# Kernel tuning notes

Hardware: AMD Instinct MI355X
Metric: run time of the kernel (lower is better)

## Reference

```python
import jax, jax.numpy as jnp
import numpy as np

C = 32                      # channels
DIMS = (8, 14, 18)          # basis_dim_per_atom for the 3 atom types
COUNTS = (8192, 8192, 4096) # number of atoms of each type


def setup_inputs() -> dict:
    key = jax.random.key(0)
    ks = iter(jax.random.split(key, 32))
    inp = {}
    N = sum(d * n for d, n in zip(DIMS, COUNTS))  # 253952 total basis rows
    inp["x"] = jax.random.normal(next(ks), (N, C), jnp.float32)
    c2 = C * C
    off = 0
    for t, (d, n) in enumerate(zip(DIMS, COUNTS)):
        rows = d * n
        # index array equivalent to the boolean atomic_number_mask for this type
        inp[f"idx{t}"] = jnp.arange(off, off + rows, dtype=jnp.int32)
        off += rows
        A = jax.random.normal(next(ks), (d, d), jnp.float32)
        inp[f"S{t}"] = 0.1 * (A + A.T)  # symmetric Coulomb/overlap matrix stand-in
        inp[f"W1_{t}"] = jax.random.normal(next(ks), (c2, c2), jnp.float32) * 0.03
        inp[f"b1_{t}"] = jnp.zeros((c2,), jnp.float32)
        inp[f"g{t}"] = jnp.ones((c2,), jnp.float32)
        inp[f"beta{t}"] = jnp.zeros((c2,), jnp.float32)
        inp[f"W2_{t}"] = jax.random.normal(next(ks), (c2, c2), jnp.float32) * 0.03
        inp[f"b2_{t}"] = jnp.zeros((c2,), jnp.float32)
    return inp


def _atom_block(y, S, W1, b1, g, beta, W2, b2):
    # y: [n_atoms, d, C]
    n = y.shape[0]
    # l2 = einsum('ij,aic,ajm->acm', S, y, y)  -> [n, C, C]
    Sy = jnp.einsum('ij,ajm->aim', S, y)
    l2 = jnp.einsum('aic,aim->acm', y, Sy)
    h = l2.reshape(n, C * C)
    # MLP: Linear -> SiLU -> LayerNorm -> Linear
    h = jax.nn.silu(h @ W1.T + b1)
    mu = jnp.mean(h, axis=-1, keepdims=True)
    var = jnp.var(h, axis=-1, keepdims=True)
    h = (h - mu) * jax.lax.rsqrt(var + 1e-5) * g + beta
    l2 = (h @ W2.T + b2).reshape(n, C, C)
    # x = x @ l2 per atom
    return jnp.einsum('aic,acm->aim', y, l2)


def reference(x, idx0, idx1, idx2,
              S0, W1_0, b1_0, g0, beta0, W2_0, b2_0,
              S1, W1_1, b1_1, g1, beta1, W2_1, b2_1,
              S2, W1_2, b1_2, g2, beta2, W2_2, b2_2):
    idxs = (idx0, idx1, idx2)
    params = ((S0, W1_0, b1_0, g0, beta0, W2_0, b2_0),
              (S1, W1_1, b1_1, g1, beta1, W2_1, b2_1),
              (S2, W1_2, b1_2, g2, beta2, W2_2, b2_2))
    for t in range(3):  # fixed small loop over atom types (structurally distinct)
        d = DIMS[t]
        y = x[idxs[t]].reshape(-1, d, C)          # gather + view per atom
        out = _atom_block(y, *params[t])          # per-type sub-module
        x = x.at[idxs[t]].set(out.reshape(-1, C)) # scatter back
    return x
```

## Files before the change

### kernel.cpp

```cpp
#include <hip/hip_runtime.h>
#include <math.h>

#define C2 1024

typedef float f32x4 __attribute__((ext_vector_type(4)));
typedef _Float16 f16x8 __attribute__((ext_vector_type(8)));
typedef unsigned short u16x8 __attribute__((ext_vector_type(8)));

__device__ __forceinline__ unsigned short f2h(float f) {
    _Float16 h = (_Float16)f;
    return __builtin_bit_cast(unsigned short, h);
}
__device__ __forceinline__ float h2f(unsigned short u) {
    return (float)__builtin_bit_cast(_Float16, u);
}

__device__ __forceinline__ void gload16(const void* g, void* l) {
    __builtin_amdgcn_global_load_lds((const __attribute__((address_space(1))) void*)g,
                                     (__attribute__((address_space(3))) void*)l,
                                     16, 0, 0);
}

__device__ __forceinline__ int type_of(int pos, int s1, int s2) {
    return (pos >= s2) ? 2 : (pos >= s1) ? 1 : 0;
}
__device__ __forceinline__ int dim_of(int t) { return (t == 0) ? 8 : (t == 1) ? 14 : 18; }

__global__ __launch_bounds__(256) void k_conv(const float* __restrict__ s0, const float* __restrict__ s1,
                                              const float* __restrict__ s2, const float* __restrict__ s3,
                                              const float* __restrict__ s4, const float* __restrict__ s5,
                                              unsigned short* __restrict__ w) {
    int mat = blockIdx.x >> 10, bb = blockIdx.x & 1023;
    const float* src = (mat == 0) ? s0 : (mat == 1) ? s1 : (mat == 2) ? s2
                       : (mat == 3) ? s3 : (mat == 4) ? s4 : s5;
    int i = (bb * 256 + threadIdx.x) * 4;
    unsigned short* dst = w + (size_t)mat * 1048576;
    float4 v = *(const float4*)(src + i);
    ushort4 h;
    h.x = f2h(v.x); h.y = f2h(v.y); h.z = f2h(v.z); h.w = f2h(v.w);
    *(ushort4*)(dst + i) = h;
}

__global__ __launch_bounds__(256) void k_l2(const float* __restrict__ x,
                                            const int* __restrict__ i0, const int* __restrict__ i1,
                                            const int* __restrict__ i2,
                                            const float* __restrict__ S0, const float* __restrict__ S1,
                                            const float* __restrict__ S2,
                                            unsigned short* __restrict__ Ah,
                                            int s1, int s2) {
    __shared__ float sS[324];
    __shared__ float sy[4][18][32];
    __shared__ float sSy[4][18][32];
    const int tid = threadIdx.x, g = tid >> 6, lane = tid & 63;
    const int a0 = blockIdx.x * 4;
    const int t = type_of(a0, s1, s2);
    const int d = dim_of(t);
    const int* idx = (t == 0) ? i0 : (t == 1) ? i1 : i2;
    const float* S = (t == 0) ? S0 : (t == 1) ? S1 : S2;
    const int start = (t == 0) ? 0 : (t == 1) ? s1 : s2;
    const int dd = d * d;
    for (int i = tid; i < dd; i += 256) sS[i] = S[i];
    const int a = a0 + g, la = a - start;
    const int nf4 = d * 8;
    for (int k = lane; k < nf4; k += 64) {
        int bi = k >> 3, f4 = (k & 7) * 4;
        int r = idx[la * d + bi];
        *(float4*)&sy[g][bi][f4] = *(const float4*)(x + (size_t)r * 32 + f4);
    }
    __syncthreads();
    for (int k = lane; k < d * 32; k += 64) {
        int i = k >> 5, m = k & 31;
        float acc = 0.f;
        for (int j = 0; j < d; ++j) acc += sS[i * d + j] * sy[g][j][m];
        sSy[g][i][m] = acc;
    }
    __syncthreads();
    const int c = lane >> 1, mb = (lane & 1) * 16;
    float acc[16];
#pragma unroll
    for (int mm = 0; mm < 16; ++mm) acc[mm] = 0.f;
    for (int i = 0; i < d; ++i) {
        float yc = sy[g][i][c];
#pragma unroll
        for (int mm = 0; mm < 16; ++mm) acc[mm] += yc * sSy[g][i][mb + mm];
    }
    u16x8 h0, h1;
#pragma unroll
    for (int mm = 0; mm < 8; ++mm) h0[mm] = f2h(acc[mm]);
#pragma unroll
    for (int mm = 0; mm < 8; ++mm) h1[mm] = f2h(acc[8 + mm]);
    size_t off = (size_t)a * C2 + lane * 16;
    *(u16x8*)(Ah + off) = h0;
    *(u16x8*)(Ah + off + 8) = h1;
}

template <int DO_SILU>
__global__ __launch_bounds__(256) void k_gemm_mfma(const unsigned short* __restrict__ A,
                                                   const unsigned short* __restrict__ W0,
                                                   const unsigned short* __restrict__ W1,
                                                   const unsigned short* __restrict__ W2,
                                                   const float* __restrict__ bias0, const float* __restrict__ bias1,
                                                   const float* __restrict__ bias2,
                                                   unsigned short* __restrict__ Out, int tb1, int tb2) {
    __shared__ short lds[8704];
    short* As = lds;
    short* Ws = lds + 4096;

    const int tid = threadIdx.x;
    const int wid = tid >> 6, lane = tid & 63;
    const int bm = blockIdx.x, bn = blockIdx.y;
    const int wr = wid >> 1, wc = wid & 1;

    const unsigned short* W; const float* bias;
    if (bm >= tb2)      { W = W2; bias = bias2; }
    else if (bm >= tb1) { W = W1; bias = bias1; }
    else                { W = W0; bias = bias0; }

    size_t gA[2], gW[2];
    int ldsoff[2];
#pragma unroll
    for (int it = 0; it < 2; ++it) {
        int L = wid * 128 + it * 64 + lane;
        int row = L >> 2, slot = L & 3;
        int sw = slot ^ ((row >> 1) & 3);
        gA[it] = (size_t)(bm * 128 + row) * C2 + sw * 8;
        gW[it] = (size_t)(bn * 128 + row) * C2 + sw * 8;
        ldsoff[it] = wid * 1024 + it * 512;
    }

    const int col = lane & 15, g = lane >> 4;
    int aoffs[4], woffs[4];
#pragma unroll
    for (int i = 0; i < 4; ++i) {
        int ra = wr * 64 + i * 16 + col;
        aoffs[i] = ra * 32 + (g ^ ((ra >> 1) & 3)) * 8;
        int rw = wc * 64 + i * 16 + col;
        woffs[i] = rw * 32 + (g ^ ((rw >> 1) & 3)) * 8;
    }

    f32x4 acc[4][4] = {};

    for (int k0 = 0; k0 < C2; k0 += 32) {
#pragma unroll
        for (int it = 0; it < 2; ++it) {
            gload16(A + gA[it] + k0, As + ldsoff[it]);
            gload16(W + gW[it] + k0, Ws + ldsoff[it]);
        }
        __syncthreads();
        f16x8 ah[4], wh[4];
#pragma unroll
        for (int i = 0; i < 4; ++i) {
            ah[i] = *(const f16x8*)(As + aoffs[i]);
            wh[i] = *(const f16x8*)(Ws + woffs[i]);
        }
#pragma unroll
        for (int mi = 0; mi < 4; ++mi)
#pragma unroll
            for (int ni = 0; ni < 4; ++ni)
                acc[mi][ni] = __builtin_amdgcn_mfma_f32_16x16x32_f16(ah[mi], wh[ni], acc[mi][ni], 0, 0, 0);
        __syncthreads();
    }

    float bv[4];
#pragma unroll
    for (int ni = 0; ni < 4; ++ni) bv[ni] = bias[bn * 128 + wc * 64 + ni * 16 + col];

#pragma unroll
    for (int hp = 0; hp < 2; ++hp) {
        __syncthreads();
#pragma unroll
        for (int mh = 0; mh < 2; ++mh) {
            int mi = hp * 2 + mh;
#pragma unroll
            for (int ni = 0; ni < 4; ++ni)
#pragma unroll
                for (int r = 0; r < 4; ++r) {
                    float v = acc[mi][ni][r] + bv[ni];
                    if (DO_SILU) v = v / (1.f + __expf(-v));
                    int row = mh * 16 + g * 4 + r;
                    int colc = wc * 64 + ni * 16 + col;
                    lds[(wr * 32 + row) * 136 + colc] = (short)f2h(v);
                }
        }
        __syncthreads();
#pragma unroll
        for (int i = 0; i < 4; ++i) {
            int ci = tid + i * 256;
            int wrp = ci >> 9, rem = ci & 511;
            int row = rem >> 4, c8 = rem & 15;
            u16x8 val = *(u16x8*)&lds[(wrp * 32 + row) * 136 + c8 * 8];
            int grow = bm * 128 + wrp * 64 + hp * 32 + row;
            int gcol = bn * 128 + c8 * 8;
            *(u16x8*)&Out[(size_t)grow * C2 + gcol] = val;
        }
    }
}

__global__ __launch_bounds__(256) void k_ln(const unsigned short* __restrict__ H,
                                            const float* __restrict__ g0, const float* __restrict__ g1,
                                            const float* __restrict__ g2,
                                            const float* __restrict__ b0, const float* __restrict__ b1,
                                            const float* __restrict__ b2,
                                            unsigned short* __restrict__ Bh,
                                            int s1, int s2) {
    const int tid = threadIdx.x, w = tid >> 6, lane = tid & 63;
    const int row = blockIdx.x * 4 + w;
    const int t = type_of(row, s1, s2);
    const float* gg = (t == 0) ? g0 : (t == 1) ? g1 : g2;
    const float* bb = (t == 0) ? b0 : (t == 1) ? b1 : b2;
    const unsigned short* rp = H + (size_t)row * C2 + lane * 16;
    u16x8 hv0 = *(const u16x8*)rp;
    u16x8 hv1 = *(const u16x8*)(rp + 8);
    float v[16];
#pragma unroll
    for (int k = 0; k < 8; ++k) v[k] = h2f(hv0[k]);
#pragma unroll
    for (int k = 0; k < 8; ++k) v[8 + k] = h2f(hv1[k]);
    float s = 0.f, s2v = 0.f;
#pragma unroll
    for (int k = 0; k < 16; ++k) { s += v[k]; s2v += v[k] * v[k]; }
#pragma unroll
    for (int off = 1; off < 64; off <<= 1) {
        s += __shfl_xor(s, off);
        s2v += __shfl_xor(s2v, off);
    }
    float mean = s * (1.f / 1024.f);
    float var = s2v * (1.f / 1024.f) - mean * mean;
    float rstd = rsqrtf(var + 1e-5f);
    u16x8 o0, o1;
#pragma unroll
    for (int q = 0; q < 4; ++q) {
        float4 gv = *(const float4*)(gg + lane * 16 + q * 4);
        float4 bv = *(const float4*)(bb + lane * 16 + q * 4);
        float r0 = (v[q * 4 + 0] - mean) * rstd * gv.x + bv.x;
        float r1 = (v[q * 4 + 1] - mean) * rstd * gv.y + bv.y;
        float r2 = (v[q * 4 + 2] - mean) * rstd * gv.z + bv.z;
        float r3 = (v[q * 4 + 3] - mean) * rstd * gv.w + bv.w;
        if (q < 2) {
            o0[q * 4 + 0] = f2h(r0); o0[q * 4 + 1] = f2h(r1);
            o0[q * 4 + 2] = f2h(r2); o0[q * 4 + 3] = f2h(r3);
        } else {
            o1[(q - 2) * 4 + 0] = f2h(r0); o1[(q - 2) * 4 + 1] = f2h(r1);
            o1[(q - 2) * 4 + 2] = f2h(r2); o1[(q - 2) * 4 + 3] = f2h(r3);
        }
    }
    unsigned short* op = Bh + (size_t)row * C2 + lane * 16;
    *(u16x8*)op = o0;
    *(u16x8*)(op + 8) = o1;
}

__global__ __launch_bounds__(256) void k_out(const float* __restrict__ x,
                                             const int* __restrict__ i0, const int* __restrict__ i1,
                                             const int* __restrict__ i2,
                                             const unsigned short* __restrict__ L,
                                             float* __restrict__ out, int s1, int s2) {
    __shared__ float sL[4][C2];
    __shared__ float sy[4][18][32];
    const int tid = threadIdx.x, g = tid >> 6, lane = tid & 63;
    const int a0 = blockIdx.x * 4;
    const int t = type_of(a0, s1, s2);
    const int d = dim_of(t);
    const int* idx = (t == 0) ? i0 : (t == 1) ? i1 : i2;
    const int start = (t == 0) ? 0 : (t == 1) ? s1 : s2;
    const int a = a0 + g, la = a - start;
    for (int k = lane; k < 128; k += 64) {
        u16x8 hv = *(const u16x8*)(L + (size_t)a * C2 + k * 8);
#pragma unroll
        for (int q = 0; q < 8; ++q) sL[g][k * 8 + q] = h2f(hv[q]);
    }
    const int nf4 = d * 8;
    for (int k = lane; k < nf4; k += 64) {
        int bi = k >> 3, f4 = (k & 7) * 4;
        int r = idx[la * d + bi];
        *(float4*)&sy[g][bi][f4] = *(const float4*)(x + (size_t)r * 32 + f4);
    }
    __syncthreads();
    for (int k = lane; k < nf4; k += 64) {
        int bi = k >> 3, m4 = (k & 7) * 4;
        float ax = 0.f, ay = 0.f, az = 0.f, aw = 0.f;
#pragma unroll
        for (int c = 0; c < 32; ++c) {
            float yv = sy[g][bi][c];
            float4 lv = *(const float4*)&sL[g][c * 32 + m4];
            ax += yv * lv.x; ay += yv * lv.y; az += yv * lv.z; aw += yv * lv.w;
        }
        int r = idx[la * d + bi];
        float4 o = {ax, ay, az, aw};
        *(float4*)(out + (size_t)r * 32 + m4) = o;
    }
}

extern "C" void kernel_launch(void* const* d_in, const int* in_sizes, int n_in,
                              void* d_out, int out_size, void* d_ws, size_t ws_size,
                              hipStream_t stream) {
    const float* x = (const float*)d_in[0];
    static const int DIMS[3] = {8, 14, 18};
    static const int NATOMS[3] = {8192, 8192, 4096};
    const size_t MiB = 1ull << 20;
    const int BIG = 0x40000000;
    char* p = (char*)d_ws;

    const int* idxs[3]; const float* Ss[3]; const float* W1s[3]; const float* b1s[3];
    const float* gs[3]; const float* bes[3]; const float* W2s[3]; const float* b2s[3];
    for (int t = 0; t < 3; ++t) {
        idxs[t] = (const int*)d_in[1 + 8 * t];
        Ss[t] = (const float*)d_in[2 + 8 * t];
        W1s[t] = (const float*)d_in[3 + 8 * t];
        b1s[t] = (const float*)d_in[4 + 8 * t];
        gs[t] = (const float*)d_in[5 + 8 * t];
        bes[t] = (const float*)d_in[6 + 8 * t];
        W2s[t] = (const float*)d_in[7 + 8 * t];
        b2s[t] = (const float*)d_in[8 + 8 * t];
    }
    float* outp = (float*)d_out;

    if (ws_size >= 92 * MiB) {
        unsigned short* w = (unsigned short*)p;
        unsigned short* Ah = (unsigned short*)(p + 12 * MiB);
        unsigned short* H = (unsigned short*)(p + 52 * MiB);
        k_conv<<<6 * 1024, 256, 0, stream>>>(W1s[0], W2s[0], W1s[1], W2s[1], W1s[2], W2s[2], w);
        k_l2<<<5120, 256, 0, stream>>>(x, idxs[0], idxs[1], idxs[2], Ss[0], Ss[1], Ss[2],
                                       Ah, 8192, 16384);
        dim3 gg(160, 8);
        k_gemm_mfma<1><<<gg, 256, 0, stream>>>(Ah,
            w + 0 * 1048576, w + 2 * 1048576, w + 4 * 1048576,
            b1s[0], b1s[1], b1s[2], H, 64, 128);
        k_ln<<<5120, 256, 0, stream>>>(H, gs[0], gs[1], gs[2], bes[0], bes[1], bes[2],
                                       Ah, 8192, 16384);
        k_gemm_mfma<0><<<gg, 256, 0, stream>>>(Ah,
            w + 1 * 1048576, w + 3 * 1048576, w + 5 * 1048576,
            b2s[0], b2s[1], b2s[2], H, 64, 128);
        k_out<<<5120, 256, 0, stream>>>(x, idxs[0], idxs[1], idxs[2], H, outp, 8192, 16384);
    } else {
        unsigned short* wt = (unsigned short*)p;
        char* dyn = p + 4 * MiB;
        for (int t = 0; t < 3; ++t) {
            int n = NATOMS[t], d = DIMS[t];
            size_t fullneed = 4 * MiB + (size_t)n * 4096;
            int nch = (ws_size >= fullneed) ? 1 : 2;
            int cm = n / nch;
            unsigned short* Ah = (unsigned short*)dyn;
            unsigned short* Hbuf = (unsigned short*)(dyn + (size_t)cm * 2048);
            int ss1 = (t == 0) ? BIG : 0;
            int ss2 = (t == 2) ? 0 : BIG;
            k_conv<<<2 * 1024, 256, 0, stream>>>(W1s[t], W2s[t], W1s[t], W1s[t], W1s[t], W1s[t], wt);
            for (int ch = 0; ch < nch; ++ch) {
                const int* idxc = idxs[t] + (size_t)(ch * cm) * d;
                k_l2<<<cm / 4, 256, 0, stream>>>(x, idxc, idxc, idxc, Ss[t], Ss[t], Ss[t],
                                                 Ah, ss1, ss2);
                dim3 g1(cm / 128, 8);
                k_gemm_mfma<1><<<g1, 256, 0, stream>>>(Ah,
                    wt + 0, wt + 0, wt + 0,
                    b1s[t], b1s[t], b1s[t], Hbuf, BIG, BIG);
                k_ln<<<cm / 4, 256, 0, stream>>>(Hbuf, gs[t], gs[t], gs[t], bes[t], bes[t], bes[t],
                                                 Ah, ss1, ss2);
                k_gemm_mfma<0><<<g1, 256, 0, stream>>>(Ah,
                    wt + 1048576, wt + 1048576, wt + 1048576,
                    b2s[t], b2s[t], b2s[t], Hbuf, BIG, BIG);
                k_out<<<cm / 4, 256, 0, stream>>>(x, idxc, idxc, idxc, Hbuf, outp, ss1, ss2);
            }
        }
    }
    (void)in_sizes; (void)n_in; (void)out_size;
}
```

Measured before the change: 329.9 us.

## Double-buffer GEMM LDS tiles and fuse weight conversion into front kernel

```diff
diff --git a/kernel.cpp b/kernel.cpp
--- a/kernel.cpp
+++ b/kernel.cpp
@@ -26,33 +26,37 @@
 }
 __device__ __forceinline__ int dim_of(int t) { return (t == 0) ? 8 : (t == 1) ? 14 : 18; }
 
-__global__ __launch_bounds__(256) void k_conv(const float* __restrict__ s0, const float* __restrict__ s1,
-                                              const float* __restrict__ s2, const float* __restrict__ s3,
-                                              const float* __restrict__ s4, const float* __restrict__ s5,
-                                              unsigned short* __restrict__ w) {
-    int mat = blockIdx.x >> 10, bb = blockIdx.x & 1023;
-    const float* src = (mat == 0) ? s0 : (mat == 1) ? s1 : (mat == 2) ? s2
-                       : (mat == 3) ? s3 : (mat == 4) ? s4 : s5;
-    int i = (bb * 256 + threadIdx.x) * 4;
-    unsigned short* dst = w + (size_t)mat * 1048576;
-    float4 v = *(const float4*)(src + i);
-    ushort4 h;
-    h.x = f2h(v.x); h.y = f2h(v.y); h.z = f2h(v.z); h.w = f2h(v.w);
-    *(ushort4*)(dst + i) = h;
-}
-
-__global__ __launch_bounds__(256) void k_l2(const float* __restrict__ x,
-                                            const int* __restrict__ i0, const int* __restrict__ i1,
-                                            const int* __restrict__ i2,
-                                            const float* __restrict__ S0, const float* __restrict__ S1,
-                                            const float* __restrict__ S2,
-                                            unsigned short* __restrict__ Ah,
-                                            int s1, int s2) {
+__global__ __launch_bounds__(256) void k_front(const float* __restrict__ x,
+                                               const int* __restrict__ i0, const int* __restrict__ i1,
+                                               const int* __restrict__ i2,
+                                               const float* __restrict__ S0, const float* __restrict__ S1,
+                                               const float* __restrict__ S2,
+                                               unsigned short* __restrict__ Ah,
+                                               int s1, int s2,
+                                               const float* __restrict__ w0, const float* __restrict__ w1,
+                                               const float* __restrict__ w2, const float* __restrict__ w3,
+                                               const float* __restrict__ w4, const float* __restrict__ w5,
+                                               unsigned short* __restrict__ w,
+                                               int nconv) {
     __shared__ float sS[324];
     __shared__ float sy[4][18][32];
     __shared__ float sSy[4][18][32];
-    const int tid = threadIdx.x, g = tid >> 6, lane = tid & 63;
-    const int a0 = blockIdx.x * 4;
+    const int tid = threadIdx.x;
+    if ((int)blockIdx.x < nconv) {
+        int mat = blockIdx.x >> 10, bb = blockIdx.x & 1023;
+        const float* src = (mat == 0) ? w0 : (mat == 1) ? w1 : (mat == 2) ? w2
+                           : (mat == 3) ? w3 : (mat == 4) ? w4 : w5;
+        int i = (bb * 256 + tid) * 4;
+        unsigned short* dst = w + (size_t)mat * 1048576;
+        float4 v = *(const float4*)(src + i);
+        ushort4 h;
+        h.x = f2h(v.x); h.y = f2h(v.y); h.z = f2h(v.z); h.w = f2h(v.w);
+        *(ushort4*)(dst + i) = h;
+        return;
+    }
+    const int bid = blockIdx.x - nconv;
+    const int g = tid >> 6, lane = tid & 63;
+    const int a0 = bid * 4;
     const int t = type_of(a0, s1, s2);
     const int d = dim_of(t);
     const int* idx = (t == 0) ? i0 : (t == 1) ? i1 : i2;
@@ -102,9 +106,7 @@
                                                    const float* __restrict__ bias0, const float* __restrict__ bias1,
                                                    const float* __restrict__ bias2,
                                                    unsigned short* __restrict__ Out, int tb1, int tb2) {
-    __shared__ short lds[8704];
-    short* As = lds;
-    short* Ws = lds + 4096;
+    __shared__ short lds[16384];
 
     const int tid = threadIdx.x;
     const int wid = tid >> 6, lane = tid & 63;
@@ -140,18 +142,28 @@
 
     f32x4 acc[4][4] = {};
 
+#pragma unroll
+    for (int it = 0; it < 2; ++it) {
+        gload16(A + gA[it], lds + ldsoff[it]);
+        gload16(W + gW[it], lds + 4096 + ldsoff[it]);
+    }
+    __syncthreads();
+
+    int base = 0;
     for (int k0 = 0; k0 < C2; k0 += 32) {
-#pragma unroll
-        for (int it = 0; it < 2; ++it) {
-            gload16(A + gA[it] + k0, As + ldsoff[it]);
-            gload16(W + gW[it] + k0, Ws + ldsoff[it]);
-        }
-        __syncthreads();
+        int nbase = base ^ 8192;
+        if (k0 + 32 < C2) {
+#pragma unroll
+            for (int it = 0; it < 2; ++it) {
+                gload16(A + gA[it] + k0 + 32, lds + nbase + ldsoff[it]);
+                gload16(W + gW[it] + k0 + 32, lds + nbase + 4096 + ldsoff[it]);
+            }
+        }
         f16x8 ah[4], wh[4];
 #pragma unroll
         for (int i = 0; i < 4; ++i) {
-            ah[i] = *(const f16x8*)(As + aoffs[i]);
-            wh[i] = *(const f16x8*)(Ws + woffs[i]);
+            ah[i] = *(const f16x8*)(lds + base + aoffs[i]);
+            wh[i] = *(const f16x8*)(lds + base + 4096 + woffs[i]);
         }
 #pragma unroll
         for (int mi = 0; mi < 4; ++mi)
@@ -159,6 +171,7 @@
             for (int ni = 0; ni < 4; ++ni)
                 acc[mi][ni] = __builtin_amdgcn_mfma_f32_16x16x32_f16(ah[mi], wh[ni], acc[mi][ni], 0, 0, 0);
         __syncthreads();
+        base = nbase;
     }
 
     float bv[4];
@@ -318,9 +331,10 @@
         unsigned short* w = (unsigned short*)p;
         unsigned short* Ah = (unsigned short*)(p + 12 * MiB);
         unsigned short* H = (unsigned short*)(p + 52 * MiB);
-        k_conv<<<6 * 1024, 256, 0, stream>>>(W1s[0], W2s[0], W1s[1], W2s[1], W1s[2], W2s[2], w);
-        k_l2<<<5120, 256, 0, stream>>>(x, idxs[0], idxs[1], idxs[2], Ss[0], Ss[1], Ss[2],
-                                       Ah, 8192, 16384);
+        k_front<<<6144 + 5120, 256, 0, stream>>>(x, idxs[0], idxs[1], idxs[2],
+                                                 Ss[0], Ss[1], Ss[2], Ah, 8192, 16384,
+                                                 W1s[0], W2s[0], W1s[1], W2s[1], W1s[2], W2s[2],
+                                                 w, 6144);
         dim3 gg(160, 8);
         k_gemm_mfma<1><<<gg, 256, 0, stream>>>(Ah,
             w + 0 * 1048576, w + 2 * 1048576, w + 4 * 1048576,
@@ -343,11 +357,13 @@
             unsigned short* Hbuf = (unsigned short*)(dyn + (size_t)cm * 2048);
             int ss1 = (t == 0) ? BIG : 0;
             int ss2 = (t == 2) ? 0 : BIG;
-            k_conv<<<2 * 1024, 256, 0, stream>>>(W1s[t], W2s[t], W1s[t], W1s[t], W1s[t], W1s[t], wt);
             for (int ch = 0; ch < nch; ++ch) {
                 const int* idxc = idxs[t] + (size_t)(ch * cm) * d;
-                k_l2<<<cm / 4, 256, 0, stream>>>(x, idxc, idxc, idxc, Ss[t], Ss[t], Ss[t],
-                                                 Ah, ss1, ss2);
+                int nconv = (ch == 0) ? 2048 : 0;
+                k_front<<<nconv + cm / 4, 256, 0, stream>>>(x, idxc, idxc, idxc,
+                                                            Ss[t], Ss[t], Ss[t], Ah, ss1, ss2,
+                                                            W1s[t], W2s[t], W1s[t], W1s[t], W1s[t], W1s[t],
+                                                            wt, nconv);
                 dim3 g1(cm / 128, 8);
                 k_gemm_mfma<1><<<g1, 256, 0, stream>>>(Ah,
                     wt + 0, wt + 0, wt + 0,
```

New measurement: 322.9 us. -2.1%, faster.
